# Performance work log

Hardware: AMD Instinct MI355X
Metric: run time of the kernel (lower is better)

## Reference

```python
import jax, jax.numpy as jnp
import numpy as np

D_MODEL, D_STATE, D_CONV, EXPAND, HEADDIM = 256, 16, 4, 2, 16
D_INNER = EXPAND * D_MODEL            # 512
NHEADS = D_INNER // HEADDIM           # 32
CONV_DIM = D_INNER + 2 * D_STATE      # 544 (ngroups=1)
D_IN_PROJ = 2 * D_INNER + 2 * D_STATE + NHEADS  # 1088
BATCH, SEQLEN = 8, 4096


def setup_inputs() -> dict:
    key = jax.random.key(0)
    ks = jax.random.split(key, 8)
    u = jax.random.normal(ks[0], (BATCH, SEQLEN, D_MODEL), jnp.float32)
    W_in = jax.random.normal(ks[1], (D_MODEL, D_IN_PROJ), jnp.float32) * 0.02
    conv_w = jax.random.normal(ks[2], (CONV_DIM, 1, D_CONV), jnp.float32) * 0.2
    conv_b = jnp.zeros((CONV_DIM,), jnp.float32)
    # dt_bias init: inverse-softplus of dt ~ Uniform in log-space [dt_min, dt_max]
    dt = jnp.exp(jax.random.uniform(ks[3], (NHEADS,), jnp.float32)
                 * (np.log(0.1) - np.log(0.001)) + np.log(0.001))
    dt = jnp.clip(dt, 1e-4, None)
    dt_bias = dt + jnp.log(-jnp.expm1(-dt))
    A_log = jnp.log(jax.random.uniform(ks[4], (NHEADS,), jnp.float32, 1.0, 16.0))
    D = jnp.ones((NHEADS,), jnp.float32)
    norm_w = jnp.ones((D_INNER,), jnp.float32)
    W_out = jax.random.normal(ks[5], (D_INNER, D_MODEL), jnp.float32) * 0.02
    return dict(u=u, W_in=W_in, conv_w=conv_w, conv_b=conv_b, dt_bias=dt_bias,
                A_log=A_log, D=D, norm_w=norm_w, W_out=W_out)


def _mamba2_forward(u, W_in, conv_w, conv_b, dt_bias, A_log, D, norm_w, W_out):
    batch, seqlen, _ = u.shape
    zxbcdt = u @ W_in                                   # (B, L, 2*d_inner + 2*N + H)
    z = zxbcdt[..., :D_INNER]                           # gate
    xBC = zxbcdt[..., D_INNER:2 * D_INNER + 2 * D_STATE]
    dt = jax.nn.softplus(zxbcdt[..., -NHEADS:] + dt_bias)  # (B, L, H)
    # causal depthwise conv1d over time + SiLU
    xc = jnp.transpose(xBC, (0, 2, 1))                  # (B, C, L)
    xc = jax.lax.conv_general_dilated(
        xc, conv_w, window_strides=(1,), padding=[(D_CONV - 1, 0)],
        feature_group_count=CONV_DIM, dimension_numbers=('NCH', 'OIH', 'NCH'))
    xBC = jax.nn.silu(jnp.transpose(xc, (0, 2, 1)) + conv_b)
    x = xBC[..., :D_INNER].reshape(batch, seqlen, NHEADS, HEADDIM)  # (B,L,H,P)
    Bm = xBC[..., D_INNER:D_INNER + D_STATE]            # (B, L, N), ngroups=1
    Cm = xBC[..., D_INNER + D_STATE:]                   # (B, L, N)
    A = -jnp.exp(A_log)                                 # (H,)
    dA = jnp.exp(dt * A)                                # (B, L, H) decay per step

    # selective scan: h_t = dA_t * h_{t-1} + dt_t * (B_t outer x_t); y_t = C_t . h_t
    def step(h, inp):
        da_t, dt_t, b_t, x_t, c_t = inp
        h = da_t[:, :, None, None] * h + jnp.einsum('bh,bn,bhp->bhpn', dt_t, b_t, x_t)
        y_t = jnp.einsum('bhpn,bn->bhp', h, c_t)
        return h, y_t

    h0 = jnp.zeros((batch, NHEADS, HEADDIM, D_STATE), u.dtype)
    xs = (jnp.moveaxis(dA, 1, 0), jnp.moveaxis(dt, 1, 0),
          jnp.moveaxis(Bm, 1, 0), jnp.moveaxis(x, 1, 0), jnp.moveaxis(Cm, 1, 0))
    _, ys = jax.lax.scan(step, h0, xs)                  # ys: (L, B, H, P)
    y = jnp.moveaxis(ys, 0, 1) + D[None, None, :, None] * x
    y = y.reshape(batch, seqlen, D_INNER)
    # gated RMSNorm (norm_before_gate=False): normalize(y * silu(z)) * weight
    t = y * jax.nn.silu(z)
    t = t * jax.lax.rsqrt(jnp.mean(t * t, axis=-1, keepdims=True) + 1e-5) * norm_w
    return t @ W_out


def reference(u, W_in, conv_w, conv_b, dt_bias, A_log, D, norm_w, W_out):
    return _mamba2_forward(u, W_in, conv_w, conv_b, dt_bias, A_log, D, norm_w, W_out)
```

## Files before the change

### kernel.cpp

```cpp
#include <hip/hip_runtime.h>
#include <hip/hip_bf16.h>
#include <math.h>

#define BATCH   8
#define SEQLEN  4096
#define DMODEL  256
#define DSTATE  16
#define NHEADS  32
#define HEADDIM 16
#define DINNER  512
#define CONVDIM 544
#define DINPROJ 1088
#define NROWS   (BATCH*SEQLEN)
#define CHUNK   64
#define NCH     (SEQLEN/CHUNK)

typedef __attribute__((ext_vector_type(8))) short short8;
typedef __attribute__((ext_vector_type(8))) unsigned short ushort8;
typedef __attribute__((ext_vector_type(4))) float f32x4;

__device__ __forceinline__ float bfu2f(unsigned short u){
  union { float f; unsigned int i; } x; x.i = ((unsigned int)u) << 16; return x.f;
}
__device__ __forceinline__ unsigned short f2bfu(float f){
  union { float f; unsigned int u; } v; v.f = f;
  v.u += 0x7fffu + ((v.u >> 16) & 1u);
  return (unsigned short)(v.u >> 16);
}

__global__ __launch_bounds__(256) void k_cast_u(const float* __restrict__ u, unsigned short* __restrict__ ub){
  int i = blockIdx.x*256 + threadIdx.x;
  float4 v = reinterpret_cast<const float4*>(u)[i];
  ushort4 o; o.x=f2bfu(v.x); o.y=f2bfu(v.y); o.z=f2bfu(v.z); o.w=f2bfu(v.w);
  reinterpret_cast<ushort4*>(ub)[i] = o;
}

__global__ __launch_bounds__(256) void k_transpose_cast(const float* __restrict__ W, unsigned short* __restrict__ WT, int K, int N){
  int idx = blockIdx.x*256 + threadIdx.x;
  if (idx >= N*K) return;
  int n = idx / K, k = idx - n*K;
  WT[idx] = f2bfu(W[(size_t)k*N + n]);
}

template<int EPI, int WC, int K, int NYL2>
__global__ __launch_bounds__(WC*128) void k_gemm(
    const unsigned short* __restrict__ A,
    const unsigned short* __restrict__ BT,
    int nbase,
    unsigned short* __restrict__ oz,
    unsigned short* __restrict__ oxbc,
    float* __restrict__ odtraw,
    float* __restrict__ of32, int Nout)
{
  constexpr int BN      = WC*32;
  constexpr int THREADS = WC*128;
  constexpr int NAI     = 1024/THREADS;
  constexpr int NBI     = (BN*8)/THREADS;
  __shared__ uint4 lds[(128 + BN)*8];
  const int tid = threadIdx.x;
  const int l   = tid & 63;
  const int w   = tid >> 6;
  const int wr  = w & 1, wc = w >> 1;
  int bx, by;
  if (NYL2 == 0){ bx = blockIdx.x; by = 0; }
  else {
    int flat = blockIdx.x;
    int xcd = flat & 7;
    int grp = flat >> 3;
    by = grp & ((1 << NYL2) - 1);
    bx = (grp >> NYL2)*8 + xcd;
  }
  const int bm0 = bx * 128;
  const int bn0 = nbase + by * BN;
  const int fr  = l & 15, kq = l >> 4;
  f32x4 acc[4][2] = {};
  const int nK = K >> 6;
  for (int kt = 0; kt < nK; ++kt){
    const int k0 = kt << 6;
    #pragma unroll
    for (int i = 0; i < NAI; ++i){
      int idx = tid + i*THREADS;
      int row = idx >> 3, slot = idx & 7;
      uint4 v = *reinterpret_cast<const uint4*>(A + (size_t)(bm0+row)*K + k0 + slot*8);
      lds[row*8 + (slot ^ (row & 7))] = v;
    }
    #pragma unroll
    for (int i = 0; i < NBI; ++i){
      int idx = tid + i*THREADS;
      int row = idx >> 3, slot = idx & 7;
      uint4 v = *reinterpret_cast<const uint4*>(BT + (size_t)(bn0+row)*K + k0 + slot*8);
      lds[1024 + row*8 + (slot ^ (row & 7))] = v;
    }
    __syncthreads();
    short8 bf[2][2];
    #pragma unroll
    for (int kk = 0; kk < 2; ++kk){
      #pragma unroll
      for (int nf = 0; nf < 2; ++nf){
        int rb = wc*32 + nf*16 + fr;
        bf[kk][nf] = *reinterpret_cast<const short8*>(&lds[1024 + rb*8 + ((kk*4 + kq) ^ (rb & 7))]);
      }
    }
    #pragma unroll
    for (int mf = 0; mf < 4; ++mf){
      int ra = wr*64 + mf*16 + fr;
      #pragma unroll
      for (int kk = 0; kk < 2; ++kk){
        short8 af = *reinterpret_cast<const short8*>(&lds[ra*8 + ((kk*4 + kq) ^ (ra & 7))]);
        #pragma unroll
        for (int nf = 0; nf < 2; ++nf)
          acc[mf][nf] = __builtin_amdgcn_mfma_f32_16x16x32_bf16(af, bf[kk][nf], acc[mf][nf], 0, 0, 0);
      }
    }
    __syncthreads();
  }
  #pragma unroll
  for (int mf = 0; mf < 4; ++mf){
    #pragma unroll
    for (int nf = 0; nf < 2; ++nf){
      #pragma unroll
      for (int r = 0; r < 4; ++r){
        int m = bm0 + wr*64 + mf*16 + kq*4 + r;
        int n = bn0 + wc*32 + nf*16 + fr;
        float v = acc[mf][nf][r];
        if (EPI == 1){
          if (n < DINNER)                 oz[(size_t)m*DINNER + n] = f2bfu(v);
          else if (n < DINNER + CONVDIM)  oxbc[(size_t)m*CONVDIM + (n - DINNER)] = f2bfu(v);
          else                            odtraw[(size_t)m*NHEADS + (n - DINNER - CONVDIM)] = v;
        } else {
          of32[(size_t)m*Nout + n] = v;
        }
      }
    }
  }
}

__global__ __launch_bounds__(256) void k_convbc(const unsigned short* __restrict__ xbc,
                                                const float* __restrict__ cw,
                                                const float* __restrict__ cb,
                                                float* __restrict__ bco){
  const int tid = threadIdx.x;
  const int j = tid & 31;
  const int rt = tid >> 5;
  const int r0 = blockIdx.x*64 + rt*8;
  const int ch = 512 + j;
  const int tloc = r0 & (SEQLEN-1);
  float wv0 = cw[ch*4+0], wv1 = cw[ch*4+1], wv2 = cw[ch*4+2], wv3 = cw[ch*4+3];
  const float bias = cb[ch];
  float xr[11];
  #pragma unroll
  for (int k = 0; k < 11; ++k){
    int r = r0 - 3 + k;
    xr[k] = (tloc - 3 + k < 0) ? 0.f : bfu2f(xbc[(size_t)r*CONVDIM + ch]);
  }
  #pragma unroll
  for (int i = 0; i < 8; ++i){
    float acc = fmaf(wv0, xr[i], fmaf(wv1, xr[i+1], fmaf(wv2, xr[i+2], fmaf(wv3, xr[i+3], bias))));
    bco[(size_t)(r0+i)*32 + j] = acc / (1.f + __expf(-acc));
  }
}

__global__ __launch_bounds__(256) void k_dtda(const float* __restrict__ dtraw,
                                              const float* __restrict__ dt_bias,
                                              const float* __restrict__ A_log,
                                              float* __restrict__ dt_o,
                                              float* __restrict__ dA_o){
  int i = blockIdx.x*256 + threadIdx.x;
  int h = i & (NHEADS-1);
  float x = dtraw[i] + dt_bias[h];
  float dt = (x > 20.f) ? x : log1pf(expf(x));
  dt_o[i] = dt;
  dA_o[i] = expf(-expf(A_log[h]) * dt);
}

__global__ __launch_bounds__(256,4) void k_scan1(
    const unsigned short* __restrict__ xbc, const float* __restrict__ bc,
    const float* __restrict__ dta, const float* __restrict__ daa,
    const float* __restrict__ cwv, const float* __restrict__ cbv,
    const float* __restrict__ Dv,
    unsigned short* __restrict__ ylb, float* __restrict__ st, float* __restrict__ Pp)
{
  __shared__ float sBC[65*32];
  __shared__ float sdt[65*16];
  __shared__ float sda[65*16];
  const int tid = threadIdx.x;
  const int bid = blockIdx.x;
  const int qh = bid & 1;
  const int c  = (bid >> 1) & (NCH-1);
  const int b  = bid >> 7;
  const int w  = tid >> 6;
  const int l  = tid & 63;
  const int q  = qh*4 + w;
  const int hh = l >> 4, p = l & 15;
  const int h  = q*4 + hh;
  const size_t row0 = (size_t)b*SEQLEN + (size_t)c*CHUNK;
  const int xoff = q*64 + l;
  {
    const float* src = bc + row0*32;
    #pragma unroll
    for (int i = 0; i < 2; ++i){
      int idx = tid + i*256;
      *reinterpret_cast<float4*>(&sBC[idx*4]) = *reinterpret_cast<const float4*>(src + (size_t)idx*4);
    }
  }
  {
    int t = tid >> 2, g = (tid & 3)*4;
    *reinterpret_cast<float4*>(&sdt[t*16+g]) =
      *reinterpret_cast<const float4*>(dta + (row0+t)*NHEADS + qh*16 + g);
    *reinterpret_cast<float4*>(&sda[t*16+g]) =
      *reinterpret_cast<const float4*>(daa + (row0+t)*NHEADS + qh*16 + g);
  }
  const float cw0 = cwv[xoff*4+0], cw1 = cwv[xoff*4+1], cw2 = cwv[xoff*4+2], cw3 = cwv[xoff*4+3];
  const float cb0 = cbv[xoff];
  const float Dh = Dv[h];
  const int dIdx = w*4 + hh;
  float wA, wB, wC;
  if (c == 0){ wA = wB = wC = 0.f; }
  else {
    wA = bfu2f(xbc[(row0-3)*CONVDIM + xoff]);
    wB = bfu2f(xbc[(row0-2)*CONVDIM + xoff]);
    wC = bfu2f(xbc[(row0-1)*CONVDIM + xoff]);
  }
  float xq0 = bfu2f(xbc[(row0+0)*CONVDIM + xoff]);
  float xq1 = bfu2f(xbc[(row0+1)*CONVDIM + xoff]);
  float xq2 = bfu2f(xbc[(row0+2)*CONVDIM + xoff]);
  float xq3 = bfu2f(xbc[(row0+3)*CONVDIM + xoff]);
  __syncthreads();
  float BA[32], BB[32];
  #pragma unroll
  for (int k = 0; k < 8; ++k)
    *reinterpret_cast<float4*>(&BA[4*k]) = *reinterpret_cast<const float4*>(&sBC[4*k]);
  float dtA = sdt[dIdx], daA = sda[dIdx];
  float dtB, daB;
  float hs[16];
  #pragma unroll
  for (int n = 0; n < 16; ++n) hs[n] = 0.f;
  float cum = 1.f;

#define S1STEP(CUR, NXT, DTC, DAC, DTN, DAN, XQ, T) {                          \
    const int t_ = (T);                                                        \
    _Pragma("unroll")                                                          \
    for (int k = 0; k < 8; ++k)                                                \
      *reinterpret_cast<float4*>(&NXT[4*k]) =                                  \
        *reinterpret_cast<const float4*>(&sBC[(t_+1)*32 + 4*k]);               \
    DTN = sdt[(t_+1)*16 + dIdx]; DAN = sda[(t_+1)*16 + dIdx];                  \
    float xnew = bfu2f(xbc[(row0 + t_ + 4)*CONVDIM + xoff]);                   \
    float xc = fmaf(cw0, wA, fmaf(cw1, wB, fmaf(cw2, wC, fmaf(cw3, XQ, cb0))));\
    wA = wB; wB = wC; wC = XQ; XQ = xnew;                                      \
    float xs = xc / (1.f + __expf(-xc));                                       \
    float dx = DTC * xs;                                                       \
    float y_ = 0.f;                                                            \
    _Pragma("unroll")                                                          \
    for (int n = 0; n < 16; ++n) hs[n] = fmaf(DAC, hs[n], dx*CUR[n]);          \
    _Pragma("unroll")                                                          \
    for (int n = 0; n < 16; ++n) y_ = fmaf(hs[n], CUR[16+n], y_);              \
    cum *= DAC;                                                                \
    ylb[(row0 + t_)*DINNER + xoff] = f2bfu(y_ + Dh*xs);                        \
  }

  for (int T = 0; T < CHUNK; T += 4){
    S1STEP(BA, BB, dtA, daA, dtB, daB, xq0, T+0);
    S1STEP(BB, BA, dtB, daB, dtA, daA, xq1, T+1);
    S1STEP(BA, BB, dtA, daA, dtB, daB, xq2, T+2);
    S1STEP(BB, BA, dtB, daB, dtA, daA, xq3, T+3);
  }
#undef S1STEP
  float* sp = st + (((size_t)(b*NHEADS + h)*NCH + c)*16 + p)*16;
  #pragma unroll
  for (int k = 0; k < 4; ++k)
    *reinterpret_cast<float4*>(sp + 4*k) = make_float4(hs[4*k], hs[4*k+1], hs[4*k+2], hs[4*k+3]);
  if (p == 0) Pp[((size_t)b*NHEADS + h)*NCH + c] = cum;
}

__global__ __launch_bounds__(64) void k_scan2(float* __restrict__ st, const float* __restrict__ Pp){
  const int bh = blockIdx.x;
  const int l = threadIdx.x;
  float* sb = st + (size_t)bh*NCH*256 + l*4;
  const float* pb = Pp + (size_t)bh*NCH;
  float4 carry = make_float4(0.f,0.f,0.f,0.f);
  float4 Hb[4]; float Pb[4];
  #pragma unroll
  for (int i = 0; i < 4; ++i){
    Hb[i] = *reinterpret_cast<const float4*>(sb + (size_t)i*256);
    Pb[i] = pb[i];
  }
  for (int c0 = 0; c0 < NCH; c0 += 4){
    #pragma unroll
    for (int i = 0; i < 4; ++i){
      const int cc = c0 + i;
      float4 Hc = Hb[i]; float Pc = Pb[i];
      if (cc + 4 < NCH){
        Hb[i] = *reinterpret_cast<const float4*>(sb + (size_t)(cc+4)*256);
        Pb[i] = pb[cc+4];
      }
      *reinterpret_cast<float4*>(sb + (size_t)cc*256) = carry;
      carry.x = fmaf(Pc, carry.x, Hc.x);
      carry.y = fmaf(Pc, carry.y, Hc.y);
      carry.z = fmaf(Pc, carry.z, Hc.z);
      carry.w = fmaf(Pc, carry.w, Hc.w);
    }
  }
}

__global__ __launch_bounds__(512) void k_scan3g(
    const unsigned short* __restrict__ ylb, const float* __restrict__ bc,
    const float* __restrict__ daa, const float* __restrict__ st,
    unsigned short* __restrict__ zbf, const float* __restrict__ nw)
{
  __shared__ float sC[65*16];
  __shared__ float sda[65*32];
  __shared__ float sred[2][4][8];
  const int tid = threadIdx.x;
  const int bid = blockIdx.x;
  const int half = bid & 1;
  const int c = (bid >> 1) & (NCH-1);
  const int b = bid >> 7;
  const int T0 = half*32;
  const int w = tid >> 6;
  const int l = tid & 63;
  const int hh = l >> 4, p = l & 15;
  const int h = w*4 + hh;
  const size_t row0 = (size_t)b*SEQLEN + (size_t)c*CHUNK;
  const int xoff = w*64 + l;
  if (tid < 256){
    int t = tid >> 2, g = (tid & 3)*4;
    *reinterpret_cast<float4*>(&sC[t*16+g]) =
      *reinterpret_cast<const float4*>(bc + (row0+t)*32 + 16 + g);
  } else {
    int j = tid - 256;
    #pragma unroll
    for (int kk = 0; kk < 2; ++kk){
      int idx = j*2 + kk;
      int t = idx >> 3, g = (idx & 7)*4;
      *reinterpret_cast<float4*>(&sda[t*32+g]) =
        *reinterpret_cast<const float4*>(daa + (row0+t)*NHEADS + g);
    }
  }
  float hi[16];
  {
    const float* sp = st + (((size_t)(b*NHEADS + h)*NCH + c)*16 + p)*16;
    #pragma unroll
    for (int k = 0; k < 4; ++k){
      float4 v = *reinterpret_cast<const float4*>(sp + 4*k);
      hi[4*k] = v.x; hi[4*k+1] = v.y; hi[4*k+2] = v.z; hi[4*k+3] = v.w;
    }
  }
  const float nwv = nw[xoff];
  float yq0 = bfu2f(ylb[(row0+T0+0)*DINNER + xoff]);
  float yq1 = bfu2f(ylb[(row0+T0+1)*DINNER + xoff]);
  float yq2 = bfu2f(ylb[(row0+T0+2)*DINNER + xoff]);
  float yq3 = bfu2f(ylb[(row0+T0+3)*DINNER + xoff]);
  float zq0 = bfu2f(zbf[(row0+T0+0)*DINNER + xoff]);
  float zq1 = bfu2f(zbf[(row0+T0+1)*DINNER + xoff]);
  float zq2 = bfu2f(zbf[(row0+T0+2)*DINNER + xoff]);
  float zq3 = bfu2f(zbf[(row0+T0+3)*DINNER + xoff]);
  __syncthreads();
  float cum = 1.f;
  for (int t = 0; t < T0; ++t) cum *= sda[t*32 + h];
  float CA[16], CB[16];
  #pragma unroll
  for (int k = 0; k < 4; ++k)
    *reinterpret_cast<float4*>(&CA[4*k]) = *reinterpret_cast<const float4*>(&sC[T0*16 + 4*k]);
  float daA = sda[T0*32 + h], daB;

#define S3STEP(CUR, NXT, DAC, DAN, YQ, ZQ, TV, PS, T) {                        \
    const int t_ = (T);                                                        \
    _Pragma("unroll")                                                          \
    for (int k = 0; k < 4; ++k)                                                \
      *reinterpret_cast<float4*>(&NXT[4*k]) =                                  \
        *reinterpret_cast<const float4*>(&sC[(t_+1)*16 + 4*k]);                \
    DAN = sda[(t_+1)*32 + h];                                                  \
    float ynew = bfu2f(ylb[(row0 + t_ + 4)*DINNER + xoff]);                    \
    float znew = bfu2f(zbf[(row0 + t_ + 4)*DINNER + xoff]);                    \
    cum *= DAC;                                                                \
    float corr = 0.f;                                                          \
    _Pragma("unroll")                                                          \
    for (int n = 0; n < 16; ++n) corr = fmaf(hi[n], CUR[n], corr);             \
    float yv = YQ + cum*corr;                                                  \
    float sg = ZQ / (1.f + __expf(-ZQ));                                       \
    TV = yv * sg; PS = TV*TV;                                                  \
    YQ = ynew; ZQ = znew;                                                      \
  }

  for (int T = T0; T < T0 + 32; T += 4){
    float tv0, tv1, tv2, tv3, ps0, ps1, ps2, ps3;
    S3STEP(CA, CB, daA, daB, yq0, zq0, tv0, ps0, T+0);
    S3STEP(CB, CA, daB, daA, yq1, zq1, tv1, ps1, T+1);
    S3STEP(CA, CB, daA, daB, yq2, zq2, tv2, ps2, T+2);
    S3STEP(CB, CA, daB, daA, yq3, zq3, tv3, ps3, T+3);
    #pragma unroll
    for (int m = 1; m <= 32; m <<= 1){
      ps0 += __shfl_xor(ps0, m, 64);
      ps1 += __shfl_xor(ps1, m, 64);
      ps2 += __shfl_xor(ps2, m, 64);
      ps3 += __shfl_xor(ps3, m, 64);
    }
    const int gb = (T >> 2) & 1;
    if (l == 0){
      sred[gb][0][w] = ps0; sred[gb][1][w] = ps1;
      sred[gb][2][w] = ps2; sred[gb][3][w] = ps3;
    }
    __syncthreads();
    float ss[4];
    #pragma unroll
    for (int i = 0; i < 4; ++i){
      float4 ra = *reinterpret_cast<const float4*>(&sred[gb][i][0]);
      float4 rb = *reinterpret_cast<const float4*>(&sred[gb][i][4]);
      ss[i] = (ra.x+ra.y)+(ra.z+ra.w)+((rb.x+rb.y)+(rb.z+rb.w));
    }
    unsigned short* zp = zbf + (row0 + T)*DINNER + xoff;
    zp[0*DINNER] = f2bfu(tv0 * rsqrtf(ss[0]*(1.f/DINNER) + 1e-5f) * nwv);
    zp[1*DINNER] = f2bfu(tv1 * rsqrtf(ss[1]*(1.f/DINNER) + 1e-5f) * nwv);
    zp[2*DINNER] = f2bfu(tv2 * rsqrtf(ss[2]*(1.f/DINNER) + 1e-5f) * nwv);
    zp[3*DINNER] = f2bfu(tv3 * rsqrtf(ss[3]*(1.f/DINNER) + 1e-5f) * nwv);
  }
#undef S3STEP
}

extern "C" void kernel_launch(void* const* d_in, const int* in_sizes, int n_in,
                              void* d_out, int out_size, void* d_ws, size_t ws_size,
                              hipStream_t stream)
{
  const float* u       = (const float*)d_in[0];
  const float* W_in    = (const float*)d_in[1];
  const float* conv_w  = (const float*)d_in[2];
  const float* conv_b  = (const float*)d_in[3];
  const float* dt_bias = (const float*)d_in[4];
  const float* A_log   = (const float*)d_in[5];
  const float* Dvec    = (const float*)d_in[6];
  const float* norm_w  = (const float*)d_in[7];
  const float* W_out   = (const float*)d_in[8];
  float* out = (float*)d_out;
  char* ws = (char*)d_ws;

  unsigned short* ubf   = (unsigned short*)(ws + 0);
  float* chst           = (float*)(ws + 0);
  unsigned short* wintT = (unsigned short*)(ws + 16777216);
  unsigned short* woutT = (unsigned short*)(ws + 17334272);
  unsigned short* zbf   = (unsigned short*)(ws + 17596416);
  unsigned short* xbcbf = (unsigned short*)(ws + 51150848);
  float* dtraw          = (float*)(ws + 86802432);
  float* Pp             = dtraw;
  unsigned short* ylb   = (unsigned short*)(ws + 90996736);
  float* convoBC        = (float*)(ws + 158105600);
  float* dtq            = (float*)(ws + 162299904);
  float* daq            = (float*)(ws + 166494208);

  k_cast_u<<<NROWS*DMODEL/1024, 256, 0, stream>>>(u, ubf);
  k_transpose_cast<<<(DINPROJ*DMODEL+255)/256, 256, 0, stream>>>(W_in, wintT, DMODEL, DINPROJ);
  k_transpose_cast<<<(DINNER*DMODEL+255)/256, 256, 0, stream>>>(W_out, woutT, DINNER, DMODEL);

  k_gemm<1,4,DMODEL,3><<<(NROWS/128)*8, 512, 0, stream>>>(ubf, wintT, 0, zbf, xbcbf, dtraw, nullptr, 0);
  k_gemm<1,2,DMODEL,0><<<NROWS/128, 256, 0, stream>>>(ubf, wintT, 1024, zbf, xbcbf, dtraw, nullptr, 0);

  k_convbc<<<NROWS/64, 256, 0, stream>>>(xbcbf, conv_w, conv_b, convoBC);
  k_dtda<<<NROWS*NHEADS/256, 256, 0, stream>>>(dtraw, dt_bias, A_log, dtq, daq);

  k_scan1<<<BATCH*2*NCH, 256, 0, stream>>>(xbcbf, convoBC, dtq, daq, conv_w, conv_b, Dvec,
                                           ylb, chst, Pp);
  k_scan2<<<BATCH*NHEADS, 64, 0, stream>>>(chst, Pp);
  k_scan3g<<<BATCH*NCH*2, 512, 0, stream>>>(ylb, convoBC, daq, chst, zbf, norm_w);

  k_gemm<2,4,DINNER,1><<<(NROWS/128)*2, 512, 0, stream>>>(zbf, woutT, 0, nullptr, nullptr, nullptr, out, DMODEL);
}
```

Before: 174.9 us.

## Split scan3 chunk into quarters and batch RMSNorm reduction per block

After: 175.2 us. Within noise of the previous version (+0.1%).

```diff
diff --git a/kernel.cpp b/kernel.cpp
--- a/kernel.cpp
+++ b/kernel.cpp
@@ -307,15 +307,15 @@
     const float* __restrict__ daa, const float* __restrict__ st,
     unsigned short* __restrict__ zbf, const float* __restrict__ nw)
 {
-  __shared__ float sC[65*16];
-  __shared__ float sda[65*32];
-  __shared__ float sred[2][4][8];
+  __shared__ float sC[16*16];
+  __shared__ float sda[64*32];
+  __shared__ float sred[16][8];
   const int tid = threadIdx.x;
   const int bid = blockIdx.x;
-  const int half = bid & 1;
-  const int c = (bid >> 1) & (NCH-1);
-  const int b = bid >> 7;
-  const int T0 = half*32;
+  const int qt = bid & 3;
+  const int c = (bid >> 2) & (NCH-1);
+  const int b = bid >> 8;
+  const int T0 = qt*16;
   const int w = tid >> 6;
   const int l = tid & 63;
   const int hh = l >> 4, p = l & 15;
@@ -323,9 +323,8 @@
   const size_t row0 = (size_t)b*SEQLEN + (size_t)c*CHUNK;
   const int xoff = w*64 + l;
   if (tid < 256){
-    int t = tid >> 2, g = (tid & 3)*4;
-    *reinterpret_cast<float4*>(&sC[t*16+g]) =
-      *reinterpret_cast<const float4*>(bc + (row0+t)*32 + 16 + g);
+    int t = tid >> 4, col = tid & 15;
+    sC[t*16 + col] = bc[(row0 + T0 + t)*32 + 16 + col];
   } else {
     int j = tid - 256;
     #pragma unroll
@@ -346,75 +345,45 @@
     }
   }
   const float nwv = nw[xoff];
-  float yq0 = bfu2f(ylb[(row0+T0+0)*DINNER + xoff]);
-  float yq1 = bfu2f(ylb[(row0+T0+1)*DINNER + xoff]);
-  float yq2 = bfu2f(ylb[(row0+T0+2)*DINNER + xoff]);
-  float yq3 = bfu2f(ylb[(row0+T0+3)*DINNER + xoff]);
-  float zq0 = bfu2f(zbf[(row0+T0+0)*DINNER + xoff]);
-  float zq1 = bfu2f(zbf[(row0+T0+1)*DINNER + xoff]);
-  float zq2 = bfu2f(zbf[(row0+T0+2)*DINNER + xoff]);
-  float zq3 = bfu2f(zbf[(row0+T0+3)*DINNER + xoff]);
+  float yv[16], zv[16];
+  #pragma unroll
+  for (int i = 0; i < 16; ++i){
+    yv[i] = bfu2f(ylb[(row0 + T0 + i)*DINNER + xoff]);
+    zv[i] = bfu2f(zbf[(row0 + T0 + i)*DINNER + xoff]);
+  }
   __syncthreads();
   float cum = 1.f;
   for (int t = 0; t < T0; ++t) cum *= sda[t*32 + h];
-  float CA[16], CB[16];
-  #pragma unroll
-  for (int k = 0; k < 4; ++k)
-    *reinterpret_cast<float4*>(&CA[4*k]) = *reinterpret_cast<const float4*>(&sC[T0*16 + 4*k]);
-  float daA = sda[T0*32 + h], daB;
-
-#define S3STEP(CUR, NXT, DAC, DAN, YQ, ZQ, TV, PS, T) {                        \
-    const int t_ = (T);                                                        \
-    _Pragma("unroll")                                                          \
-    for (int k = 0; k < 4; ++k)                                                \
-      *reinterpret_cast<float4*>(&NXT[4*k]) =                                  \
-        *reinterpret_cast<const float4*>(&sC[(t_+1)*16 + 4*k]);                \
-    DAN = sda[(t_+1)*32 + h];                                                  \
-    float ynew = bfu2f(ylb[(row0 + t_ + 4)*DINNER + xoff]);                    \
-    float znew = bfu2f(zbf[(row0 + t_ + 4)*DINNER + xoff]);                    \
-    cum *= DAC;                                                                \
-    float corr = 0.f;                                                          \
-    _Pragma("unroll")                                                          \
-    for (int n = 0; n < 16; ++n) corr = fmaf(hi[n], CUR[n], corr);             \
-    float yv = YQ + cum*corr;                                                  \
-    float sg = ZQ / (1.f + __expf(-ZQ));                                       \
-    TV = yv * sg; PS = TV*TV;                                                  \
-    YQ = ynew; ZQ = znew;                                                      \
-  }
-
-  for (int T = T0; T < T0 + 32; T += 4){
-    float tv0, tv1, tv2, tv3, ps0, ps1, ps2, ps3;
-    S3STEP(CA, CB, daA, daB, yq0, zq0, tv0, ps0, T+0);
-    S3STEP(CB, CA, daB, daA, yq1, zq1, tv1, ps1, T+1);
-    S3STEP(CA, CB, daA, daB, yq2, zq2, tv2, ps2, T+2);
-    S3STEP(CB, CA, daB, daA, yq3, zq3, tv3, ps3, T+3);
-    #pragma unroll
-    for (int m = 1; m <= 32; m <<= 1){
-      ps0 += __shfl_xor(ps0, m, 64);
-      ps1 += __shfl_xor(ps1, m, 64);
-      ps2 += __shfl_xor(ps2, m, 64);
-      ps3 += __shfl_xor(ps3, m, 64);
-    }
-    const int gb = (T >> 2) & 1;
-    if (l == 0){
-      sred[gb][0][w] = ps0; sred[gb][1][w] = ps1;
-      sred[gb][2][w] = ps2; sred[gb][3][w] = ps3;
-    }
-    __syncthreads();
-    float ss[4];
-    #pragma unroll
-    for (int i = 0; i < 4; ++i){
-      float4 ra = *reinterpret_cast<const float4*>(&sred[gb][i][0]);
-      float4 rb = *reinterpret_cast<const float4*>(&sred[gb][i][4]);
-      ss[i] = (ra.x+ra.y)+(ra.z+ra.w)+((rb.x+rb.y)+(rb.z+rb.w));
-    }
-    unsigned short* zp = zbf + (row0 + T)*DINNER + xoff;
-    zp[0*DINNER] = f2bfu(tv0 * rsqrtf(ss[0]*(1.f/DINNER) + 1e-5f) * nwv);
-    zp[1*DINNER] = f2bfu(tv1 * rsqrtf(ss[1]*(1.f/DINNER) + 1e-5f) * nwv);
-    zp[2*DINNER] = f2bfu(tv2 * rsqrtf(ss[2]*(1.f/DINNER) + 1e-5f) * nwv);
-    zp[3*DINNER] = f2bfu(tv3 * rsqrtf(ss[3]*(1.f/DINNER) + 1e-5f) * nwv);
-  }
-#undef S3STEP
+  #pragma unroll
+  for (int i = 0; i < 16; ++i){
+    cum *= sda[(T0 + i)*32 + h];
+    float corr = 0.f;
+    #pragma unroll
+    for (int n = 0; n < 16; ++n) corr = fmaf(hi[n], sC[i*16 + n], corr);
+    float y_ = yv[i] + cum*corr;
+    float sg = zv[i] / (1.f + __expf(-zv[i]));
+    float tv = y_ * sg;
+    yv[i] = tv;
+    zv[i] = tv*tv;
+  }
+  #pragma unroll
+  for (int m = 1; m <= 32; m <<= 1){
+    #pragma unroll
+    for (int i = 0; i < 16; ++i) zv[i] += __shfl_xor(zv[i], m, 64);
+  }
+  if (l == 0){
+    #pragma unroll
+    for (int i = 0; i < 16; ++i) sred[i][w] = zv[i];
+  }
+  __syncthreads();
+  #pragma unroll
+  for (int i = 0; i < 16; ++i){
+    float4 ra = *reinterpret_cast<const float4*>(&sred[i][0]);
+    float4 rb = *reinterpret_cast<const float4*>(&sred[i][4]);
+    float ss = (ra.x+ra.y)+(ra.z+ra.w)+((rb.x+rb.y)+(rb.z+rb.w));
+    zbf[(row0 + T0 + i)*DINNER + xoff] =
+      f2bfu(yv[i] * rsqrtf(ss*(1.f/DINNER) + 1e-5f) * nwv);
+  }
 }
 
 extern "C" void kernel_launch(void* const* d_in, const int* in_sizes, int n_in,
@@ -459,7 +428,7 @@
   k_scan1<<<BATCH*2*NCH, 256, 0, stream>>>(xbcbf, convoBC, dtq, daq, conv_w, conv_b, Dvec,
                                            ylb, chst, Pp);
   k_scan2<<<BATCH*NHEADS, 64, 0, stream>>>(chst, Pp);
-  k_scan3g<<<BATCH*NCH*2, 512, 0, stream>>>(ylb, convoBC, daq, chst, zbf, norm_w);
+  k_scan3g<<<BATCH*NCH*4, 512, 0, stream>>>(ylb, convoBC, daq, chst, zbf, norm_w);
 
   k_gemm<2,4,DINNER,1><<<(NROWS/128)*2, 512, 0, stream>>>(zbf, woutT, 0, nullptr, nullptr, nullptr, out, DMODEL);
 }
```
